# Kernel optimization log

Measured on AMD Instinct MI355X. Metric: run time of the kernel, lower is better.

The kernel has to match this reference:

```python
import jax, jax.numpy as jnp
import numpy as np

# Static graph layout: B equal-sized graphs so per-graph k is constant (jit-friendly).
NUM_GRAPHS = 128
NODES_PER_GRAPH = 1024
NUM_NODES = NUM_GRAPHS * NODES_PER_GRAPH  # 131072
NUM_EDGES = NUM_NODES * 32               # 4194304
CHANNELS = 256
RATIO = 0.5
K = max(1, int(NODES_PER_GRAPH * RATIO))  # 512, matches max(1, int(count*ratio))


def setup_inputs() -> dict:
    key = jax.random.key(0)
    k0, k1, k2, k3 = jax.random.split(key, 4)
    x = jax.random.normal(k0, (NUM_NODES, CHANNELS), dtype=jnp.float32)
    edge_index = jax.random.randint(k1, (2, NUM_EDGES), 0, NUM_NODES, dtype=jnp.int64)
    batch = (jnp.arange(NUM_NODES, dtype=jnp.int64) // NODES_PER_GRAPH)
    # score MLP params: Linear(C, C) -> tanh -> Linear(C, 1)
    s = 1.0 / np.sqrt(CHANNELS)
    W1 = jax.random.uniform(k2, (CHANNELS, CHANNELS), jnp.float32, -s, s)
    b1 = jnp.zeros((CHANNELS,), jnp.float32)
    W2 = jax.random.uniform(k3, (CHANNELS, 1), jnp.float32, -s, s)
    b2 = jnp.zeros((1,), jnp.float32)
    return {"x": x, "edge_index": edge_index, "batch": batch,
            "W1": W1, "b1": b1, "W2": W2, "b2": b2}


def reference(x, edge_index, batch, W1, b1, W2, b2):
    # Note: SAGPool.forward computes a GNN score then discards it and calls
    # super().forward, which recomputes scores with the self.score MLP. The GNN
    # path is dead code (and would error in torch); the effective math is below.
    scores = (jnp.tanh(x @ W1 + b1) @ W2 + b2)[:, 0]  # [num_nodes]

    # Per-graph top-k, vectorized across all graphs (equal-sized segments).
    s = scores.reshape(NUM_GRAPHS, NODES_PER_GRAPH)
    top_s, top_i = jax.lax.top_k(s, K)  # descending per graph, matches torch.topk
    offsets = (jnp.arange(NUM_GRAPHS, dtype=top_i.dtype) * NODES_PER_GRAPH)[:, None]
    perm = (top_i + offsets).reshape(-1)  # [B*K] global indices, graphs in order

    x_pooled = x[perm]
    batch_pooled = batch[perm]
    scores_pooled = top_s.reshape(-1)

    # Edge filtering: keep edges whose both endpoints survive.
    keep = jnp.zeros((NUM_NODES,), dtype=bool).at[perm].set(True)
    row, col = edge_index
    edge_mask = keep[row] & keep[col]
    # Static-shape compaction: stable-sort kept edges to the front, pad with -1.
    order = jnp.argsort(~edge_mask, stable=True)
    edge_index_pooled = jnp.where(edge_mask[order][None, :], edge_index[:, order], -1)

    return x_pooled, edge_index_pooled, batch_pooled, perm, scores_pooled
```

## Files before the change

kernel.cpp:

```cpp
#include <hip/hip_runtime.h>
#include <hip/hip_bf16.h>

#define NG 128
#define NPG 1024
#define NN (NG * NPG)
#define NE (NN * 32)
#define CH 256
#define KSEL 512

#define CAP 128
#define EPS 0.02f

#define OUT_X      0
#define OUT_EDGE   16777216
#define OUT_BATCH  25165824
#define OUT_PERM   25231360
#define OUT_SCORES 25296896

#define WS_SCORES  0
#define WS_KEEP    524288
#define WS_COUNTS  540672
#define WS_OFFSETS 544768
#define WS_BFRAG   548864
#define WS_BIDX    679936
#define WS_BSCORE  745472
#define WS_BN      811008
#define WS_BLO     811520

typedef __attribute__((ext_vector_type(8))) short bf16x8;
typedef __attribute__((ext_vector_type(4))) float f32x4;

__device__ __forceinline__ unsigned short f2bf(float f) {
    unsigned int b = __float_as_uint(f);
    return (unsigned short)((b + 0x7fffu + ((b >> 16) & 1u)) >> 16);
}

__global__ __launch_bounds__(256)
void k_cvtW(const float* __restrict__ W1, unsigned short* __restrict__ W1b)
{
    const int t = blockIdx.x * 256 + threadIdx.x;
    const int s    = t >> 10;
    const int rem  = t & 1023;
    const int n    = rem >> 6;
    const int lane = rem & 63;
    const int kbase = s * 32 + (lane >> 4) * 8;
    const int col   = n * 16 + (lane & 15);
    unsigned short u[8];
    #pragma unroll
    for (int j = 0; j < 8; ++j)
        u[j] = f2bf(W1[(size_t)(kbase + j) * CH + col]);
    unsigned int w0 = u[0] | ((unsigned int)u[1] << 16);
    unsigned int w1 = u[2] | ((unsigned int)u[3] << 16);
    unsigned int w2 = u[4] | ((unsigned int)u[5] << 16);
    unsigned int w3 = u[6] | ((unsigned int)u[7] << 16);
    uint4 v; v.x = w0; v.y = w1; v.z = w2; v.w = w3;
    *(uint4*)&W1b[(size_t)t * 8] = v;
}

__global__ __launch_bounds__(256)
void k_mfma_scores(const float* __restrict__ x, const unsigned short* __restrict__ W1b,
                   const float* __restrict__ b1, const float* __restrict__ W2,
                   const float* __restrict__ b2, float* __restrict__ scores)
{
    __shared__ short As[8192];
    __shared__ float epi[4][32];

    const int tid = threadIdx.x;
    const int w_  = tid >> 6;
    const int l   = tid & 63;
    const int n0  = blockIdx.x * 32;

    #pragma unroll
    for (int it = 0; it < 8; ++it) {
        const int flat = it * 1024 + tid * 4;
        const int row = flat >> 8;
        const int c   = flat & 255;
        const float4 v = *(const float4*)&x[(size_t)(n0 + row) * CH + c];
        const int msub = row >> 4, r16 = row & 15;
        const int s = c >> 5, ksub = c & 31, g = ksub >> 3, j = ksub & 7;
        const int idx = msub * 4096 + s * 512 + g * 128 + r16 * 8 + j;
        uint2 p;
        p.x = f2bf(v.x) | ((unsigned int)f2bf(v.y) << 16);
        p.y = f2bf(v.z) | ((unsigned int)f2bf(v.w) << 16);
        *(uint2*)&As[idx] = p;
    }
    __syncthreads();

    f32x4 acc[2][4];
    #pragma unroll
    for (int m = 0; m < 2; ++m)
        #pragma unroll
        for (int n = 0; n < 4; ++n)
            acc[m][n] = (f32x4){0.f, 0.f, 0.f, 0.f};

    #pragma unroll
    for (int s = 0; s < 8; ++s) {
        const bf16x8 a0 = *(const bf16x8*)&As[0 * 4096 + s * 512 + l * 8];
        const bf16x8 a1 = *(const bf16x8*)&As[1 * 4096 + s * 512 + l * 8];
        #pragma unroll
        for (int ni = 0; ni < 4; ++ni) {
            const int nt = w_ * 4 + ni;
            const bf16x8 b = *(const bf16x8*)&W1b[(size_t)(s * 16 + nt) * 512 + l * 8];
            acc[0][ni] = __builtin_amdgcn_mfma_f32_16x16x32_bf16(a0, b, acc[0][ni], 0, 0, 0);
            acc[1][ni] = __builtin_amdgcn_mfma_f32_16x16x32_bf16(a1, b, acc[1][ni], 0, 0, 0);
        }
    }

    float part[8];
    #pragma unroll
    for (int i = 0; i < 8; ++i) part[i] = 0.f;
    #pragma unroll
    for (int ni = 0; ni < 4; ++ni) {
        const int col = w_ * 64 + ni * 16 + (l & 15);
        const float b1c = b1[col];
        const float w2c = W2[col];
        #pragma unroll
        for (int m = 0; m < 2; ++m)
            #pragma unroll
            for (int r = 0; r < 4; ++r)
                part[m * 4 + r] += tanhf(acc[m][ni][r] + b1c) * w2c;
    }
    #pragma unroll
    for (int off = 1; off < 16; off <<= 1)
        #pragma unroll
        for (int i = 0; i < 8; ++i)
            part[i] += __shfl_xor(part[i], off, 64);

    if ((l & 15) == 0) {
        const int gq = l >> 4;
        #pragma unroll
        for (int m = 0; m < 2; ++m)
            #pragma unroll
            for (int r = 0; r < 4; ++r)
                epi[w_][m * 16 + gq * 4 + r] = part[m * 4 + r];
    }
    __syncthreads();
    if (tid < 32)
        scores[n0 + tid] = epi[0][tid] + epi[1][tid] + epi[2][tid] + epi[3][tid] + b2[0];
}

__global__ __launch_bounds__(512)
void k_topk(const float* __restrict__ scores, float* __restrict__ out,
            unsigned int* __restrict__ keep_bits, int* __restrict__ band_idx,
            int* __restrict__ band_n, int* __restrict__ band_lo)
{
    __shared__ float sv[1024];
    __shared__ int   si[1024];
    __shared__ int   s_lo, s_hi;
    const int g = blockIdx.x;
    const int t = threadIdx.x;
    sv[t]       = scores[g * NPG + t];       si[t]       = t;
    sv[t + 512] = scores[g * NPG + t + 512]; si[t + 512] = t + 512;

    for (int size = 2; size <= 1024; size <<= 1) {
        for (int stride = size >> 1; stride > 0; stride >>= 1) {
            __syncthreads();
            const int lo = ((t & ~(stride - 1)) << 1) | (t & (stride - 1));
            const int hi = lo + stride;
            const bool dirDesc = ((lo & size) == 0);
            const float va = sv[lo], vb = sv[hi];
            const int ia = si[lo], ib = si[hi];
            const bool aB = (va > vb) || (va == vb && ia < ib);
            if (aB != dirDesc) {
                sv[lo] = vb; sv[hi] = va;
                si[lo] = ib; si[hi] = ia;
            }
        }
    }
    __syncthreads();
    if (t == 0) { s_hi = 1024; }
    __syncthreads();
    const float tau = sv[511];
    if (sv[t] <= tau + EPS && (t == 0 || sv[t - 1] > tau + EPS)) s_lo = t;
    {
        const int p2 = t + 512;
        if (sv[p2] < tau - EPS && sv[p2 - 1] >= tau - EPS) s_hi = p2;
    }
    __syncthreads();
    const int lo = s_lo;
    const int bn = min(s_hi - lo, CAP);

    const int gi = g * NPG + si[t];
    out[OUT_BATCH + g * KSEL + t] = (float)g;
    if (t < lo) {
        out[OUT_PERM   + g * KSEL + t] = (float)gi;
        out[OUT_SCORES + g * KSEL + t] = sv[t];
        atomicOr(&keep_bits[gi >> 5], 1u << (gi & 31));
    }
    if (t < CAP)
        band_idx[g * CAP + t] = (t < bn) ? si[lo + t] : 0;
    if (t == 0) { band_n[g] = bn; band_lo[g] = lo; }
}

__global__ __launch_bounds__(256, 2)
void k_rescore(const float* __restrict__ x, const float* __restrict__ W1,
               const float* __restrict__ b1, const float* __restrict__ W2,
               const float* __restrict__ b2, const int* __restrict__ band_idx,
               const int* __restrict__ band_n, float* __restrict__ band_scores)
{
    const int g = blockIdx.x >> 2;
    const int c0 = (blockIdx.x & 3) * 32;
    if (band_n[g] <= c0) return;

    __shared__ __align__(16) float W1s[16][CH];
    __shared__ __align__(16) float Xs[32][16];

    const int tid = threadIdx.x;
    const int w_  = tid >> 6;
    const int l   = tid & 63;

    int iv = 0;
    if (w_ < 2) iv = band_idx[g * CAP + c0 + w_ * 16 + (l >> 2)] & 1023;
    const float* xg = x + ((size_t)g * NPG + iv) * CH;

    const float4 b1v = *(const float4*)&b1[l * 4];
    float acc[8][4];
    #pragma unroll
    for (int n = 0; n < 8; ++n) {
        acc[n][0] = b1v.x; acc[n][1] = b1v.y; acc[n][2] = b1v.z; acc[n][3] = b1v.w;
    }

    for (int kc = 0; kc < 16; ++kc) {
        __syncthreads();
        #pragma unroll
        for (int it = 0; it < 4; ++it) {
            const float* gp = W1 + (size_t)kc * (16 * CH) + (w_ * 4 + it) * CH + l * 4;
            float* lb = &W1s[0][0] + (w_ * 4 + it) * CH;
            __builtin_amdgcn_global_load_lds(
                (const __attribute__((address_space(1))) void*)gp,
                (__attribute__((address_space(3))) void*)lb, 16, 0, 0);
        }
        if (w_ < 2) {
            const float* gp = xg + kc * 16 + (l & 3) * 4;
            float* lb = &Xs[0][0] + w_ * 256;
            __builtin_amdgcn_global_load_lds(
                (const __attribute__((address_space(1))) void*)gp,
                (__attribute__((address_space(3))) void*)lb, 16, 0, 0);
        }
        __syncthreads();

        #pragma unroll
        for (int kq = 0; kq < 4; ++kq) {
            const int k4 = kq * 4;
            const float4 wv0 = *(const float4*)&W1s[k4 + 0][l * 4];
            const float4 wv1 = *(const float4*)&W1s[k4 + 1][l * 4];
            const float4 wv2 = *(const float4*)&W1s[k4 + 2][l * 4];
            const float4 wv3 = *(const float4*)&W1s[k4 + 3][l * 4];
            #pragma unroll
            for (int n = 0; n < 8; ++n) {
                const float4 xv = *(const float4*)&Xs[w_ * 8 + n][k4];
                acc[n][0] = fmaf(xv.x, wv0.x, acc[n][0]);
                acc[n][1] = fmaf(xv.x, wv0.y, acc[n][1]);
                acc[n][2] = fmaf(xv.x, wv0.z, acc[n][2]);
                acc[n][3] = fmaf(xv.x, wv0.w, acc[n][3]);
                acc[n][0] = fmaf(xv.y, wv1.x, acc[n][0]);
                acc[n][1] = fmaf(xv.y, wv1.y, acc[n][1]);
                acc[n][2] = fmaf(xv.y, wv1.z, acc[n][2]);
                acc[n][3] = fmaf(xv.y, wv1.w, acc[n][3]);
                acc[n][0] = fmaf(xv.z, wv2.x, acc[n][0]);
                acc[n][1] = fmaf(xv.z, wv2.y, acc[n][1]);
                acc[n][2] = fmaf(xv.z, wv2.z, acc[n][2]);
                acc[n][3] = fmaf(xv.z, wv2.w, acc[n][3]);
                acc[n][0] = fmaf(xv.w, wv3.x, acc[n][0]);
                acc[n][1] = fmaf(xv.w, wv3.y, acc[n][1]);
                acc[n][2] = fmaf(xv.w, wv3.z, acc[n][2]);
                acc[n][3] = fmaf(xv.w, wv3.w, acc[n][3]);
            }
        }
    }

    const float4 w2v = *(const float4*)&W2[l * 4];
    const float  bb  = b2[0];
    float s_[8];
    #pragma unroll
    for (int n = 0; n < 8; ++n) {
        s_[n] = tanhf(acc[n][0]) * w2v.x + tanhf(acc[n][1]) * w2v.y
              + tanhf(acc[n][2]) * w2v.z + tanhf(acc[n][3]) * w2v.w;
    }
    #pragma unroll
    for (int off = 1; off < 64; off <<= 1)
        #pragma unroll
        for (int n = 0; n < 8; ++n)
            s_[n] += __shfl_xor(s_[n], off, 64);

    if (l == 0) {
        #pragma unroll
        for (int n = 0; n < 8; ++n)
            band_scores[g * CAP + c0 + w_ * 8 + n] = s_[n] + bb;
    }
}

__global__ __launch_bounds__(64)
void k_bandsel(const float* __restrict__ band_scores, const int* __restrict__ band_idx,
               const int* __restrict__ band_n, const int* __restrict__ band_lo,
               float* __restrict__ out, unsigned int* __restrict__ keep_bits)
{
    __shared__ float bs[CAP];
    __shared__ int   bi[CAP];
    const int g = blockIdx.x;
    const int t = threadIdx.x;
    const int n  = band_n[g];
    const int lo = band_lo[g];
    int needed = KSEL - lo;
    if (needed > n) needed = n;

    #pragma unroll
    for (int h = 0; h < 2; ++h) {
        const int q = t + h * 64;
        const bool valid = q < n;
        bs[q] = valid ? band_scores[g * CAP + q] : -3.402823466e+38f;
        bi[q] = valid ? band_idx[g * CAP + q] : (NPG + q);
    }
    __syncthreads();
    for (int size = 2; size <= CAP; size <<= 1) {
        for (int stride = size >> 1; stride > 0; stride >>= 1) {
            __syncthreads();
            const int lo_i = ((t & ~(stride - 1)) << 1) | (t & (stride - 1));
            const int hi_i = lo_i + stride;
            const bool dirDesc = ((lo_i & size) == 0);
            const float va = bs[lo_i], vb = bs[hi_i];
            const int ia = bi[lo_i], ib = bi[hi_i];
            const bool aB = (va > vb) || (va == vb && ia < ib);
            if (aB != dirDesc) {
                bs[lo_i] = vb; bs[hi_i] = va;
                bi[lo_i] = ib; bi[hi_i] = ia;
            }
        }
    }
    __syncthreads();
    #pragma unroll
    for (int h = 0; h < 2; ++h) {
        const int s = t + h * 64;
        if (s < needed) {
            const int li = bi[s];
            const int gi = g * NPG + li;
            out[OUT_PERM   + g * KSEL + lo + s] = (float)gi;
            out[OUT_SCORES + g * KSEL + lo + s] = bs[s];
            atomicOr(&keep_bits[gi >> 5], 1u << (gi & 31));
        }
    }
}

__global__ __launch_bounds__(256)
void k_gather(const float* __restrict__ x, const float* __restrict__ perm_f,
              float* __restrict__ out_x)
{
    const int row  = blockIdx.x * 4 + (threadIdx.x >> 6);
    const int lane = threadIdx.x & 63;
    const int pi = (int)perm_f[row];
    const float4* src = (const float4*)&x[(size_t)pi * CH];
    float4* dst = (float4*)&out_x[(size_t)row * CH];
    dst[lane] = src[lane];
}

__global__ __launch_bounds__(256)
void k_fill(float* __restrict__ out_edge)
{
    const int i = blockIdx.x * blockDim.x + threadIdx.x;
    ((float4*)out_edge)[i] = make_float4(-1.f, -1.f, -1.f, -1.f);
}

__global__ __launch_bounds__(256)
void k_edgecount(const int* __restrict__ ei, const unsigned int* __restrict__ keep_bits,
                 int* __restrict__ counts)
{
    const int t = threadIdx.x;
    const size_t base = (size_t)blockIdx.x * 4096 + (size_t)t * 16;
    const int* rowp = ei;
    const int* colp = ei + NE;
    int rv[16], cv[16];
    #pragma unroll
    for (int q = 0; q < 4; ++q) {
        int4 r4 = *(const int4*)&rowp[base + q * 4];
        int4 c4 = *(const int4*)&colp[base + q * 4];
        rv[q*4+0]=r4.x; rv[q*4+1]=r4.y; rv[q*4+2]=r4.z; rv[q*4+3]=r4.w;
        cv[q*4+0]=c4.x; cv[q*4+1]=c4.y; cv[q*4+2]=c4.z; cv[q*4+3]=c4.w;
    }
    int cnt = 0;
    #pragma unroll
    for (int q = 0; q < 16; ++q)
        cnt += (int)((keep_bits[rv[q] >> 5] >> (rv[q] & 31)) &
                     (keep_bits[cv[q] >> 5] >> (cv[q] & 31)) & 1u);

    #pragma unroll
    for (int off = 1; off < 64; off <<= 1) cnt += __shfl_xor(cnt, off, 64);
    __shared__ int wsum[4];
    if ((t & 63) == 0) wsum[t >> 6] = cnt;
    __syncthreads();
    if (t == 0) counts[blockIdx.x] = wsum[0] + wsum[1] + wsum[2] + wsum[3];
}

__global__ __launch_bounds__(1024)
void k_scan(const int* __restrict__ counts, int* __restrict__ offsets)
{
    __shared__ int tmp[1024];
    const int t = threadIdx.x;
    const int c = counts[t];
    tmp[t] = c;
    __syncthreads();
    for (int off = 1; off < 1024; off <<= 1) {
        int v = (t >= off) ? tmp[t - off] : 0;
        __syncthreads();
        tmp[t] += v;
        __syncthreads();
    }
    offsets[t] = tmp[t] - c;
}

__global__ __launch_bounds__(256)
void k_scatter(const int* __restrict__ ei, const unsigned int* __restrict__ keep_bits,
               const int* __restrict__ offsets, float* __restrict__ out_edge)
{
    const int t = threadIdx.x;
    const size_t base = (size_t)blockIdx.x * 4096 + (size_t)t * 16;
    const int* rowp = ei;
    const int* colp = ei + NE;
    int rv[16], cv[16];
    #pragma unroll
    for (int q = 0; q < 4; ++q) {
        int4 r4 = *(const int4*)&rowp[base + q * 4];
        int4 c4 = *(const int4*)&colp[base + q * 4];
        rv[q*4+0]=r4.x; rv[q*4+1]=r4.y; rv[q*4+2]=r4.z; rv[q*4+3]=r4.w;
        cv[q*4+0]=c4.x; cv[q*4+1]=c4.y; cv[q*4+2]=c4.z; cv[q*4+3]=c4.w;
    }
    unsigned m = 0; int cnt = 0;
    #pragma unroll
    for (int q = 0; q < 16; ++q) {
        const bool kk = ((keep_bits[rv[q] >> 5] >> (rv[q] & 31)) &
                         (keep_bits[cv[q] >> 5] >> (cv[q] & 31)) & 1u) != 0u;
        m |= ((unsigned)kk) << q;
        cnt += (int)kk;
    }
    const int lane = t & 63, w = t >> 6;
    int incl = cnt;
    #pragma unroll
    for (int off = 1; off < 64; off <<= 1) {
        int v = __shfl_up(incl, off, 64);
        if (lane >= off) incl += v;
    }
    __shared__ int wtot[4];
    if (lane == 63) wtot[w] = incl;
    __syncthreads();
    int wbase = 0;
    for (int i = 0; i < w; ++i) wbase += wtot[i];
    int pos = offsets[blockIdx.x] + wbase + (incl - cnt);
    #pragma unroll
    for (int q = 0; q < 16; ++q) {
        if (m & (1u << q)) {
            out_edge[pos]      = (float)rv[q];
            out_edge[NE + pos] = (float)cv[q];
            ++pos;
        }
    }
}

extern "C" void kernel_launch(void* const* d_in, const int* in_sizes, int n_in,
                              void* d_out, int out_size, void* d_ws, size_t ws_size,
                              hipStream_t stream)
{
    const float* x  = (const float*)d_in[0];
    const int*   ei = (const int*)d_in[1];
    const float* W1 = (const float*)d_in[3];
    const float* b1 = (const float*)d_in[4];
    const float* W2 = (const float*)d_in[5];
    const float* b2 = (const float*)d_in[6];

    float* out = (float*)d_out;
    char*  ws  = (char*)d_ws;
    float*          scores    = (float*)(ws + WS_SCORES);
    unsigned int*   keep_bits = (unsigned int*)(ws + WS_KEEP);
    int*            counts    = (int*)(ws + WS_COUNTS);
    int*            offsets   = (int*)(ws + WS_OFFSETS);
    unsigned short* W1b       = (unsigned short*)(ws + WS_BFRAG);
    int*            band_idx  = (int*)(ws + WS_BIDX);
    float*          band_sc   = (float*)(ws + WS_BSCORE);
    int*            band_n    = (int*)(ws + WS_BN);
    int*            band_lo   = (int*)(ws + WS_BLO);

    hipMemsetAsync(keep_bits, 0, NN / 8, stream);

    k_cvtW<<<32, 256, 0, stream>>>(W1, W1b);
    k_mfma_scores<<<NN / 32, 256, 0, stream>>>(x, W1b, b1, W2, b2, scores);
    k_topk<<<NG, 512, 0, stream>>>(scores, out, keep_bits, band_idx, band_n, band_lo);
    k_rescore<<<NG * (CAP / 32), 256, 0, stream>>>(x, W1, b1, W2, b2, band_idx, band_n, band_sc);
    k_bandsel<<<NG, 64, 0, stream>>>(band_sc, band_idx, band_n, band_lo, out, keep_bits);
    k_gather<<<(NG * KSEL) / 4, 256, 0, stream>>>(x, out + OUT_PERM, out + OUT_X);
    k_fill<<<(2 * NE) / (4 * 256), 256, 0, stream>>>(out + OUT_EDGE);
    k_edgecount<<<NE / 4096, 256, 0, stream>>>(ei, keep_bits, counts);
    k_scan<<<1, 1024, 0, stream>>>(counts, offsets);
    k_scatter<<<NE / 4096, 256, 0, stream>>>(ei, keep_bits, offsets, out + OUT_EDGE);
}
```

Measured before the change: 178.7 us.

## Enlarge score GEMM tile to 64 rows with swizzled LDS and prefetched B fragments

The MFMA scoring kernel now handles 64 nodes per block instead of 32, so each W1 fragment loaded from global memory is reused across four row subtiles. The A tile is stored in row-major LDS with an XOR swizzle to avoid bank conflicts, and the next k-step's B fragments are prefetched into registers while the current MFMAs run. tanhf is replaced by an exp-based fast tanh, and launch bounds request 3 blocks per SM. These changes use more registers and LDS per block and slightly alter tanh accuracy, which could perturb near-tie top-k ordering, though a rescore band stage exists.

```diff
diff --git a/kernel.cpp b/kernel.cpp
--- a/kernel.cpp
+++ b/kernel.cpp
@@ -35,6 +35,11 @@
     return (unsigned short)((b + 0x7fffu + ((b >> 16) & 1u)) >> 16);
 }
 
+__device__ __forceinline__ float tanh_fast(float h) {
+    const float e = __expf(2.0f * h);
+    return 1.0f - 2.0f / (e + 1.0f);
+}
+
 __global__ __launch_bounds__(256)
 void k_cvtW(const float* __restrict__ W1, unsigned short* __restrict__ W1b)
 {
@@ -49,93 +54,107 @@
     #pragma unroll
     for (int j = 0; j < 8; ++j)
         u[j] = f2bf(W1[(size_t)(kbase + j) * CH + col]);
-    unsigned int w0 = u[0] | ((unsigned int)u[1] << 16);
-    unsigned int w1 = u[2] | ((unsigned int)u[3] << 16);
-    unsigned int w2 = u[4] | ((unsigned int)u[5] << 16);
-    unsigned int w3 = u[6] | ((unsigned int)u[7] << 16);
-    uint4 v; v.x = w0; v.y = w1; v.z = w2; v.w = w3;
+    uint4 v;
+    v.x = u[0] | ((unsigned int)u[1] << 16);
+    v.y = u[2] | ((unsigned int)u[3] << 16);
+    v.z = u[4] | ((unsigned int)u[5] << 16);
+    v.w = u[6] | ((unsigned int)u[7] << 16);
     *(uint4*)&W1b[(size_t)t * 8] = v;
 }
 
-__global__ __launch_bounds__(256)
+__global__ __launch_bounds__(256, 3)
 void k_mfma_scores(const float* __restrict__ x, const unsigned short* __restrict__ W1b,
                    const float* __restrict__ b1, const float* __restrict__ W2,
                    const float* __restrict__ b2, float* __restrict__ scores)
 {
-    __shared__ short As[8192];
-    __shared__ float epi[4][32];
+    __shared__ __align__(16) short As[64 * 256];
+    __shared__ float epi[4][64];
 
     const int tid = threadIdx.x;
     const int w_  = tid >> 6;
     const int l   = tid & 63;
-    const int n0  = blockIdx.x * 32;
-
-    #pragma unroll
-    for (int it = 0; it < 8; ++it) {
+    const int n0  = blockIdx.x * 64;
+
+    #pragma unroll
+    for (int it = 0; it < 16; ++it) {
         const int flat = it * 1024 + tid * 4;
         const int row = flat >> 8;
         const int c   = flat & 255;
         const float4 v = *(const float4*)&x[(size_t)(n0 + row) * CH + c];
-        const int msub = row >> 4, r16 = row & 15;
-        const int s = c >> 5, ksub = c & 31, g = ksub >> 3, j = ksub & 7;
-        const int idx = msub * 4096 + s * 512 + g * 128 + r16 * 8 + j;
         uint2 p;
         p.x = f2bf(v.x) | ((unsigned int)f2bf(v.y) << 16);
         p.y = f2bf(v.z) | ((unsigned int)f2bf(v.w) << 16);
-        *(uint2*)&As[idx] = p;
-    }
-    __syncthreads();
-
-    f32x4 acc[2][4];
-    #pragma unroll
-    for (int m = 0; m < 2; ++m)
+        const int byte = (row * 512 + c * 2) ^ ((row & 7) << 4);
+        *(uint2*)((char*)As + byte) = p;
+    }
+    __syncthreads();
+
+    f32x4 acc[4][4];
+    #pragma unroll
+    for (int m = 0; m < 4; ++m)
         #pragma unroll
         for (int n = 0; n < 4; ++n)
             acc[m][n] = (f32x4){0.f, 0.f, 0.f, 0.f};
 
+    const unsigned short* Wl = W1b + l * 8;
+    bf16x8 bc[4], bn[4];
+    #pragma unroll
+    for (int ni = 0; ni < 4; ++ni)
+        bc[ni] = *(const bf16x8*)&Wl[(size_t)(w_ * 4 + ni) * 512];
+
     #pragma unroll
     for (int s = 0; s < 8; ++s) {
-        const bf16x8 a0 = *(const bf16x8*)&As[0 * 4096 + s * 512 + l * 8];
-        const bf16x8 a1 = *(const bf16x8*)&As[1 * 4096 + s * 512 + l * 8];
-        #pragma unroll
-        for (int ni = 0; ni < 4; ++ni) {
-            const int nt = w_ * 4 + ni;
-            const bf16x8 b = *(const bf16x8*)&W1b[(size_t)(s * 16 + nt) * 512 + l * 8];
-            acc[0][ni] = __builtin_amdgcn_mfma_f32_16x16x32_bf16(a0, b, acc[0][ni], 0, 0, 0);
-            acc[1][ni] = __builtin_amdgcn_mfma_f32_16x16x32_bf16(a1, b, acc[1][ni], 0, 0, 0);
-        }
-    }
-
-    float part[8];
-    #pragma unroll
-    for (int i = 0; i < 8; ++i) part[i] = 0.f;
+        if (s < 7) {
+            #pragma unroll
+            for (int ni = 0; ni < 4; ++ni)
+                bn[ni] = *(const bf16x8*)&Wl[(size_t)((s + 1) * 16 + w_ * 4 + ni) * 512];
+        }
+        bf16x8 a[4];
+        #pragma unroll
+        for (int m = 0; m < 4; ++m) {
+            const int row  = m * 16 + (l & 15);
+            const int byte = (row * 512 + s * 64 + ((l >> 4) * 16)) ^ ((l & 7) << 4);
+            a[m] = *(const bf16x8*)((const char*)As + byte);
+        }
+        #pragma unroll
+        for (int ni = 0; ni < 4; ++ni)
+            #pragma unroll
+            for (int m = 0; m < 4; ++m)
+                acc[m][ni] = __builtin_amdgcn_mfma_f32_16x16x32_bf16(a[m], bc[ni], acc[m][ni], 0, 0, 0);
+        #pragma unroll
+        for (int ni = 0; ni < 4; ++ni) bc[ni] = bn[ni];
+    }
+
+    float part[16];
+    #pragma unroll
+    for (int i = 0; i < 16; ++i) part[i] = 0.f;
     #pragma unroll
     for (int ni = 0; ni < 4; ++ni) {
         const int col = w_ * 64 + ni * 16 + (l & 15);
         const float b1c = b1[col];
         const float w2c = W2[col];
         #pragma unroll
-        for (int m = 0; m < 2; ++m)
+        for (int m = 0; m < 4; ++m)
             #pragma unroll
             for (int r = 0; r < 4; ++r)
-                part[m * 4 + r] += tanhf(acc[m][ni][r] + b1c) * w2c;
+                part[m * 4 + r] += tanh_fast(acc[m][ni][r] + b1c) * w2c;
     }
     #pragma unroll
     for (int off = 1; off < 16; off <<= 1)
         #pragma unroll
-        for (int i = 0; i < 8; ++i)
+        for (int i = 0; i < 16; ++i)
             part[i] += __shfl_xor(part[i], off, 64);
 
     if ((l & 15) == 0) {
         const int gq = l >> 4;
         #pragma unroll
-        for (int m = 0; m < 2; ++m)
+        for (int m = 0; m < 4; ++m)
             #pragma unroll
             for (int r = 0; r < 4; ++r)
                 epi[w_][m * 16 + gq * 4 + r] = part[m * 4 + r];
     }
     __syncthreads();
-    if (tid < 32)
+    if (tid < 64)
         scores[n0 + tid] = epi[0][tid] + epi[1][tid] + epi[2][tid] + epi[3][tid] + b2[0];
 }
 
@@ -480,7 +499,7 @@
     hipMemsetAsync(keep_bits, 0, NN / 8, stream);
 
     k_cvtW<<<32, 256, 0, stream>>>(W1, W1b);
-    k_mfma_scores<<<NN / 32, 256, 0, stream>>>(x, W1b, b1, W2, b2, scores);
+    k_mfma_scores<<<NN / 64, 256, 0, stream>>>(x, W1b, b1, W2, b2, scores);
     k_topk<<<NG, 512, 0, stream>>>(scores, out, keep_bits, band_idx, band_n, band_lo);
     k_rescore<<<NG * (CAP / 32), 256, 0, stream>>>(x, W1, b1, W2, b2, band_idx, band_n, band_sc);
     k_bandsel<<<NG, 64, 0, stream>>>(band_sc, band_idx, band_n, band_lo, out, keep_bits);
```

Result: faster. 170.1 us (-4.8%).
